# Kernel optimization log

Measured on AMD Instinct MI355X. Metric: run time of the kernel, lower is better.

The kernel has to match this reference:

```python
import jax, jax.numpy as jnp
import numpy as np

DIM = 1024
H_HEADS = 16


def setup_inputs() -> dict:
    key = jax.random.key(0)
    ks = jax.random.split(key, 12)
    h, w = 48, 80
    hw = h * w
    n_frames, n_sel = 11, 384
    wscale = 1.0 / np.sqrt(DIM).astype(np.float32)
    return {
        "feats_cur": jax.random.normal(ks[0], (1, DIM, h, w), jnp.float32),
        "ps": jax.random.normal(ks[1], (1, DIM, h, w), jnp.float32),
        "feats_ref": jax.random.normal(ks[2], (n_frames, DIM, h, w), jnp.float32),
        "ext_mem": jax.random.normal(ks[3], (24000, DIM), jnp.float32),
        "glob_cache": jax.random.normal(ks[4], (4000, DIM), jnp.float32),
        "Wq": jax.random.normal(ks[5], (DIM, DIM), jnp.float32) * wscale,
        "Wk": jax.random.normal(ks[6], (DIM, DIM), jnp.float32) * wscale,
        "Wv": jax.random.normal(ks[7], (DIM, DIM), jnp.float32) * wscale,
        "Wo": jax.random.normal(ks[8], (DIM, DIM), jnp.float32) * wscale,
        "ref_sel_idx": jax.random.randint(ks[9], (n_frames, n_sel), 0, hw, jnp.int32),
        "mem_idx": jax.random.randint(ks[10], (2000,), 0, 24000, jnp.int32),
        "glob_idx": jax.random.randint(ks[11], (2000,), 0, 4000, jnp.int32),
    }


def reference(feats_cur, ps, feats_ref, ext_mem, glob_cache, Wq, Wk, Wv, Wo,
              ref_sel_idx, mem_idx, glob_idx):
    b, dim, h, w = feats_cur.shape
    hw = h * w
    # current-frame pixels with positional encoding -> queries [hw, dim]
    q_in = (feats_cur + ps)[0].reshape(dim, hw).T
    # reference frames + ps -> [F, hw, dim], sparse randperm-style subsample via precomputed indices
    ref = (feats_ref + ps).reshape(-1, dim, hw).transpose(0, 2, 1)
    sel = jnp.take_along_axis(ref, ref_sel_idx[:, :, None], axis=1).reshape(-1, dim)
    # concat with subsampled external memory and global cache pixels
    k_in = jnp.concatenate([sel, ext_mem[mem_idx], glob_cache[glob_idx]], axis=0)  # [Nk, dim]
    dh = dim // H_HEADS
    scale = 1.0 / np.sqrt(dh).astype(np.float32)
    q = (q_in @ Wq).reshape(hw, H_HEADS, dh)
    k = (k_in @ Wk).reshape(-1, H_HEADS, dh)
    v = (k_in @ Wv).reshape(-1, H_HEADS, dh)
    logits = jnp.einsum('qhd,khd->hqk', q, k) * scale  # [H, hw, Nk]
    attn = jax.nn.softmax(logits, axis=-1)
    ctx = jnp.einsum('hqk,khd->qhd', attn, v).reshape(hw, dim)
    out = q_in + ctx @ Wo  # residual, like MEGA relation module
    # back to [1, dim, h, w] as in update_lm_pixel_with_transpose
    return out.T.reshape(1, dim, h, w)
```

## Files before the change

### kernel.cpp

```cpp
#include <hip/hip_runtime.h>

using u16 = unsigned short;
using bf16x8 = __attribute__((ext_vector_type(8))) short;
using f32x4  = __attribute__((ext_vector_type(4))) float;

#define DIM   1024
#define HW    3840
#define NSEL  4224
#define NK    8224
#define NKPAD 8320
#define NH    16
#define THR   50.0f

typedef __attribute__((address_space(1))) const unsigned GU;
typedef __attribute__((address_space(3))) unsigned LU;

__device__ __forceinline__ u16 f2bf(float x) {
    unsigned u = __float_as_uint(x);
    return (u16)((u + 0x7FFFu + ((u >> 16) & 1u)) >> 16);
}

__device__ __forceinline__ float exp2fast(float x) {
    return __builtin_amdgcn_exp2f(x);
}

__global__ void prep_kernel(const float* __restrict__ Wq, const float* __restrict__ Wk,
                            const float* __restrict__ Wv, const float* __restrict__ Wo,
                            const float* __restrict__ fc, const float* __restrict__ ps,
                            const float* __restrict__ fr, const float* __restrict__ em,
                            const float* __restrict__ gc, const int* __restrict__ sel,
                            const int* __restrict__ midx, const int* __restrict__ gidx,
                            u16* __restrict__ WT, u16* __restrict__ qin, u16* __restrict__ kin) {
    const int b = blockIdx.x;
    const int tid = threadIdx.x;
    if (b < 4096) {
        const int zz = b >> 10, yy = (b >> 5) & 31, xx = b & 31;
        const float* src = zz == 0 ? Wq : zz == 1 ? Wk : zz == 2 ? Wv : Wo;
        u16* dst = WT + (size_t)zz * DIM * DIM;
        __shared__ float t[32][33];
        const int n0 = xx * 32, k0 = yy * 32;
        const int tx = tid & 31, ty = tid >> 5;
#pragma unroll
        for (int j = 0; j < 4; ++j)
            t[ty + 8 * j][tx] = src[(size_t)(k0 + ty + 8 * j) * DIM + n0 + tx];
        __syncthreads();
#pragma unroll
        for (int j = 0; j < 4; ++j)
            dst[(size_t)(n0 + ty + 8 * j) * DIM + k0 + tx] = f2bf(t[tx][ty + 8 * j]);
    } else if (b < 7936) {
        const int bb = b - 4096;
        const int xx = bb % 120, yy = bb / 120;
        __shared__ float t[32][33];
        const int p0 = xx * 32, d0 = yy * 32;
        const int tx = tid & 31, ty = tid >> 5;
#pragma unroll
        for (int j = 0; j < 4; ++j) {
            int d = d0 + ty + 8 * j;
            t[ty + 8 * j][tx] = fc[(size_t)d * HW + p0 + tx] + ps[(size_t)d * HW + p0 + tx];
        }
        __syncthreads();
#pragma unroll
        for (int j = 0; j < 4; ++j)
            qin[(size_t)(p0 + ty + 8 * j) * DIM + d0 + tx] = f2bf(t[tx][ty + 8 * j]);
    } else {
        const int row = b - 7936;
        u16* dst = kin + (size_t)row * DIM;
        const int t = tid;
        if (row < NSEL) {
            const int f = row / 384;
            const int idx = sel[row];
            const float* base = fr + (size_t)f * DIM * HW + idx;
#pragma unroll
            for (int j = 0; j < 4; ++j) {
                int d = t + 256 * j;
                dst[d] = f2bf(base[(size_t)d * HW] + ps[(size_t)d * HW + idx]);
            }
        } else if (row < NSEL + 2000) {
            const float* src = em + (size_t)midx[row - NSEL] * DIM;
#pragma unroll
            for (int j = 0; j < 4; ++j) { int d = t + 256 * j; dst[d] = f2bf(src[d]); }
        } else if (row < NK) {
            const float* src = gc + (size_t)gidx[row - (NSEL + 2000)] * DIM;
#pragma unroll
            for (int j = 0; j < 4; ++j) { int d = t + 256 * j; dst[d] = f2bf(src[d]); }
        } else {
#pragma unroll
            for (int j = 0; j < 4; ++j) dst[t + 256 * j] = 0;
        }
    }
}

__device__ __forceinline__ void gemm_bt_body(const u16* __restrict__ A,
                                             const u16* __restrict__ B,
                                             void* __restrict__ Cout,
                                             const float* __restrict__ r1,
                                             const float* __restrict__ r2,
                                             int ldc, int mode, float scale,
                                             int bx, int by) {
    __shared__ __align__(16) u16 As[2][128 * 64];
    __shared__ __align__(16) u16 Bs[2][128 * 64];
    const int tid = threadIdx.x;
    const int l = tid & 63;
    const int wv = tid >> 6;
    const int wr = (wv >> 1) * 64, wc = (wv & 1) * 64;
    const int g = l >> 4, lo = l & 15;
    const size_t bm = (size_t)by * 128, bn = (size_t)bx * 128;
    const f32x4 fzero = {0.f, 0.f, 0.f, 0.f};

    f32x4 acc[4][4];
#pragma unroll
    for (int i = 0; i < 4; ++i)
#pragma unroll
        for (int j = 0; j < 4; ++j) acc[i][j] = fzero;

#define GSTAGE(BUF, KT)                                                                         \
    {                                                                                           \
        const int k0_ = (KT) * 64;                                                              \
        _Pragma("unroll") for (int q = 0; q < 4; ++q) {                                         \
            const int idx = q * 256 + tid;                                                      \
            const int row = idx >> 3, c8 = idx & 7;                                             \
            const int scol = (c8 ^ (row & 7)) * 8;                                              \
            const int dbase = q * 2048 + wv * 512;                                              \
            __builtin_amdgcn_global_load_lds((GU*)(A + (bm + row) * DIM + k0_ + scol),          \
                                             (LU*)&As[BUF][dbase], 16, 0, 0);                   \
            __builtin_amdgcn_global_load_lds((GU*)(B + (bn + row) * DIM + k0_ + scol),          \
                                             (LU*)&Bs[BUF][dbase], 16, 0, 0);                   \
        }                                                                                       \
    }

#define GCOMPUTE(BUF)                                                                           \
    {                                                                                           \
        _Pragma("unroll") for (int ks = 0; ks < 2; ++ks) {                                      \
            bf16x8 af[4], bfv[4];                                                               \
            _Pragma("unroll") for (int mi = 0; mi < 4; ++mi) {                                  \
                const int row = wr + mi * 16 + lo;                                              \
                const int sw = (ks * 4 + g) ^ (row & 7);                                        \
                af[mi] = *(const bf16x8*)(&As[BUF][row * 64 + sw * 8]);                         \
            }                                                                                   \
            _Pragma("unroll") for (int ni = 0; ni < 4; ++ni) {                                  \
                const int row = wc + ni * 16 + lo;                                              \
                const int sw = (ks * 4 + g) ^ (row & 7);                                        \
                bfv[ni] = *(const bf16x8*)(&Bs[BUF][row * 64 + sw * 8]);                        \
            }                                                                                   \
            _Pragma("unroll") for (int mi = 0; mi < 4; ++mi)                                    \
                _Pragma("unroll") for (int ni = 0; ni < 4; ++ni)                                \
                    acc[mi][ni] = __builtin_amdgcn_mfma_f32_16x16x32_bf16(af[mi], bfv[ni], acc[mi][ni], 0, 0, 0); \
        }                                                                                       \
    }

    GSTAGE(0, 0)
    asm volatile("s_waitcnt vmcnt(0)" ::: "memory");
    __syncthreads();

#pragma unroll 1
    for (int kt = 0; kt < 16; kt += 2) {
        GSTAGE(1, kt + 1)
        GCOMPUTE(0)
        asm volatile("s_waitcnt vmcnt(0)" ::: "memory");
        __syncthreads();
        if (kt + 2 < 16) GSTAGE(0, kt + 2)
        GCOMPUTE(1)
        asm volatile("s_waitcnt vmcnt(0)" ::: "memory");
        __syncthreads();
    }
#undef GCOMPUTE
#undef GSTAGE

    if (mode == 0) {
        u16* C = (u16*)Cout;
#pragma unroll
        for (int mi = 0; mi < 4; ++mi)
#pragma unroll
            for (int ni = 0; ni < 4; ++ni)
#pragma unroll
                for (int r = 0; r < 4; ++r) {
                    size_t m = bm + wr + mi * 16 + g * 4 + r;
                    size_t n = bn + wc + ni * 16 + lo;
                    C[m * (size_t)ldc + n] = f2bf(acc[mi][ni][r] * scale);
                }
    } else if (mode == 2) {
        u16* C = (u16*)Cout;
#pragma unroll
        for (int mi = 0; mi < 4; ++mi)
#pragma unroll
            for (int ni = 0; ni < 4; ++ni)
#pragma unroll
                for (int r = 0; r < 4; ++r) {
                    size_t m = bm + wr + mi * 16 + g * 4 + r;
                    size_t n = bn + wc + ni * 16 + lo;
                    size_t o = (n >> 6) * ((size_t)NKPAD * 64) + m * 64 + (n & 63);
                    C[o] = f2bf(acc[mi][ni][r] * scale);
                }
    } else {
        float* C = (float*)Cout;
#pragma unroll
        for (int mi = 0; mi < 4; ++mi)
#pragma unroll
            for (int ni = 0; ni < 4; ++ni)
#pragma unroll
                for (int r = 0; r < 4; ++r) {
                    size_t m = bm + wr + mi * 16 + g * 4 + r;
                    size_t n = bn + wc + ni * 16 + lo;
                    size_t o = m * (size_t)ldc + n;
                    C[o] = acc[mi][ni][r] + r1[o] + r2[o];
                }
    }
}

__global__ __launch_bounds__(256, 2) void proj_kernel(const u16* __restrict__ qin,
                                                      const u16* __restrict__ kin,
                                                      const u16* __restrict__ WT,
                                                      u16* __restrict__ Qp,
                                                      u16* __restrict__ Kp,
                                                      u16* __restrict__ Vt) {
    const int b = blockIdx.x;
    if (b < 240) {
        gemm_bt_body(qin, WT, Qp, nullptr, nullptr, 1024, 0, 0.18033688f, b % 8, b / 8);
    } else if (b < 760) {
        const int bb = b - 240;
        gemm_bt_body(kin, WT + 1048576, Kp, nullptr, nullptr, 1024, 2, 1.0f, bb % 8, bb / 8);
    } else {
        const int bb = b - 760;
        gemm_bt_body(WT + 2097152, kin, Vt, nullptr, nullptr, NKPAD, 0, 1.0f, bb % 65, bb / 65);
    }
}

__global__ __launch_bounds__(256, 2) void outproj_kernel(const u16* __restrict__ WTo,
                                                         const u16* __restrict__ ctx,
                                                         float* __restrict__ out,
                                                         const float* __restrict__ fc,
                                                         const float* __restrict__ ps) {
    gemm_bt_body(WTo, ctx, out, fc, ps, HW, 1, 1.0f, blockIdx.x, blockIdx.y);
}

__global__ __launch_bounds__(256, 4) void attn_kernel(const u16* __restrict__ Q,
                                                      const u16* __restrict__ Kh,
                                                      const u16* __restrict__ Vt,
                                                      u16* __restrict__ ctx) {
    __shared__ __align__(16) u16 Kst[2][2][2048];
    __shared__ __align__(16) u16 Vst[2][2][2048];
    __shared__ float mlb[2][2][32][2];
    __shared__ float mbuf2[2][32][20];
    const int h = blockIdx.x;
    const int tid = threadIdx.x;
    const int l = tid & 63, wv = tid >> 6;
    const int qh = wv & 1, kh = wv >> 1;
    const int g = l >> 4, lo = l & 15;
    const int hoff = h * 64;
    const int qw = blockIdx.y * 64 + qh * 32;
    const f32x4 fzero = {0.f, 0.f, 0.f, 0.f};
    const int sig = (lo >> 2) * 8 + (lo & 3);
    const int W0 = kh * 128;
    const int nw = 128 + kh;

    const u16* Ksrc = Kh + (size_t)h * NKPAD * 64;
    const u16* Vsrc = Vt + (size_t)hoff * NKPAD;

    bf16x8 qa[2][2];
#pragma unroll
    for (int mi = 0; mi < 2; ++mi)
#pragma unroll
        for (int ks = 0; ks < 2; ++ks)
            qa[mi][ks] = *(const bf16x8*)(Q + (size_t)(qw + mi * 16 + lo) * DIM + hoff + ks * 32 + g * 8);

    f32x4 acc[2][4];
#pragma unroll
    for (int mi = 0; mi < 2; ++mi)
#pragma unroll
        for (int ni = 0; ni < 4; ++ni) acc[mi][ni] = fzero;
    float mrow[2] = {-1e30f, -1e30f};
    float lsum[2] = {0.f, 0.f};
    float pmax[2] = {-1e30f, -1e30f};

#define STAGE32(BUF, IT)                                                                        \
    {                                                                                           \
        const int kk_ = (W0 + (IT)) * 32;                                                       \
        _Pragma("unroll") for (int jj = 0; jj < 2; ++jj) {                                      \
            const int j = qh * 2 + jj;                                                          \
            const int rk = j * 8 + (l >> 3);                                                    \
            const int hkk = (rk & 3) | (((rk >> 3) & 1) << 2);                                  \
            const u16* gK = Ksrc + (size_t)(kk_ + rk) * 64 + (((l & 7) ^ hkk) * 8);             \
            __builtin_amdgcn_global_load_lds((GU*)gK, (LU*)&Kst[kh][BUF][j * 512], 16, 0, 0);   \
            const int xu = (l & 7) ^ (l >> 3);                                                  \
            const int dv = 2 * rk + (xu >> 2);                                                  \
            const u16* gV = Vsrc + (size_t)dv * NKPAD + kk_ + ((xu & 3) * 8);                   \
            __builtin_amdgcn_global_load_lds((GU*)gV, (LU*)&Vst[kh][BUF][j * 512], 16, 0, 0);   \
        }                                                                                       \
    }

#define COMPUTE32(BUF)                                                                          \
    {                                                                                           \
        bf16x8 kf0, kf1, kf2, kf3;                                                              \
        {                                                                                       \
            const int r0_ = sig, r1_ = sig + 4;                                                 \
            const int h0_ = (r0_ & 3) | (((r0_ >> 3) & 1) << 2);                                \
            const int h1_ = (r1_ & 3) | (((r1_ >> 3) & 1) << 2);                                \
            kf0 = *(const bf16x8*)(&Kst[kh][BUF][r0_ * 64 + ((0 + g) ^ h0_) * 8]);              \
            kf1 = *(const bf16x8*)(&Kst[kh][BUF][r0_ * 64 + ((4 + g) ^ h0_) * 8]);              \
            kf2 = *(const bf16x8*)(&Kst[kh][BUF][r1_ * 64 + ((0 + g) ^ h1_) * 8]);              \
            kf3 = *(const bf16x8*)(&Kst[kh][BUF][r1_ * 64 + ((4 + g) ^ h1_) * 8]);              \
        }                                                                                       \
        f32x4 S0[2], S1[2];                                                                     \
        _Pragma("unroll") for (int mi = 0; mi < 2; ++mi) {                                      \
            f32x4 s_ = __builtin_amdgcn_mfma_f32_16x16x32_bf16(kf0, qa[mi][0], fzero, 0, 0, 0); \
            S0[mi] = __builtin_amdgcn_mfma_f32_16x16x32_bf16(kf1, qa[mi][1], s_, 0, 0, 0);      \
            f32x4 t_ = __builtin_amdgcn_mfma_f32_16x16x32_bf16(kf2, qa[mi][0], fzero, 0, 0, 0); \
            S1[mi] = __builtin_amdgcn_mfma_f32_16x16x32_bf16(kf3, qa[mi][1], t_, 0, 0, 0);      \
        }                                                                                       \
        _Pragma("unroll") for (int mi = 0; mi < 2; ++mi) {                                      \
            float a_ = fmaxf(fmaxf(S0[mi][0], S0[mi][1]), fmaxf(S0[mi][2], S0[mi][3]));         \
            float b_ = fmaxf(fmaxf(S1[mi][0], S1[mi][1]), fmaxf(S1[mi][2], S1[mi][3]));         \
            pmax[mi] = fmaxf(pmax[mi], fmaxf(a_, b_));                                          \
        }                                                                                       \
        if (__any(fmaxf(pmax[0] - mrow[0], pmax[1] - mrow[1]) > THR)) {                         \
            _Pragma("unroll") for (int mi = 0; mi < 2; ++mi) {                                  \
                float v = pmax[mi];                                                             \
                v = fmaxf(v, __shfl_xor(v, 16));                                                \
                v = fmaxf(v, __shfl_xor(v, 32));                                                \
                float mn = fmaxf(mrow[mi], v);                                                  \
                float fct = exp2fast(mrow[mi] - mn);                                            \
                mrow[mi] = mn;                                                                  \
                lsum[mi] *= fct;                                                                \
                _Pragma("unroll") for (int r = 0; r < 4; ++r) {                                 \
                    float fr_ = __shfl(fct, g * 4 + r);                                         \
                    _Pragma("unroll") for (int ni = 0; ni < 4; ++ni) acc[mi][ni][r] *= fr_;     \
                }                                                                               \
            }                                                                                   \
        }                                                                                       \
        bf16x8 vb[4];                                                                           \
        _Pragma("unroll") for (int ni = 0; ni < 4; ++ni) {                                      \
            const int R_ = ni * 8 + (lo >> 1);                                                  \
            const int ck_ = (((lo & 1) * 4 + g) ^ (lo >> 1)) * 8;                               \
            vb[ni] = *(const bf16x8*)(&Vst[kh][BUF][R_ * 64 + ck_]);                            \
        }                                                                                       \
        _Pragma("unroll") for (int mi = 0; mi < 2; ++mi) {                                      \
            float p0 = exp2fast(S0[mi][0] - mrow[mi]);                                          \
            float p1 = exp2fast(S0[mi][1] - mrow[mi]);                                          \
            float p2 = exp2fast(S0[mi][2] - mrow[mi]);                                          \
            float p3 = exp2fast(S0[mi][3] - mrow[mi]);                                          \
            float p4 = exp2fast(S1[mi][0] - mrow[mi]);                                          \
            float p5 = exp2fast(S1[mi][1] - mrow[mi]);                                          \
            float p6 = exp2fast(S1[mi][2] - mrow[mi]);                                          \
            float p7 = exp2fast(S1[mi][3] - mrow[mi]);                                          \
            lsum[mi] += ((p0 + p1) + (p2 + p3)) + ((p4 + p5) + (p6 + p7));                      \
            union { unsigned u[4]; bf16x8 v; } pu;                                              \
            asm("v_cvt_pk_bf16_f32 %0, %1, %2" : "=v"(pu.u[0]) : "v"(p0), "v"(p1));             \
            asm("v_cvt_pk_bf16_f32 %0, %1, %2" : "=v"(pu.u[1]) : "v"(p2), "v"(p3));             \
            asm("v_cvt_pk_bf16_f32 %0, %1, %2" : "=v"(pu.u[2]) : "v"(p4), "v"(p5));             \
            asm("v_cvt_pk_bf16_f32 %0, %1, %2" : "=v"(pu.u[3]) : "v"(p6), "v"(p7));             \
            _Pragma("unroll") for (int ni = 0; ni < 4; ++ni)                                    \
                acc[mi][ni] = __builtin_amdgcn_mfma_f32_16x16x32_bf16(pu.v, vb[ni], acc[mi][ni], 0, 0, 0); \
        }                                                                                       \
    }

    STAGE32(0, 0)
    asm volatile("s_waitcnt vmcnt(0)" ::: "memory");
    __syncthreads();

#pragma unroll 1
    for (int it = 0; it + 1 < nw; it += 2) {
        STAGE32(1, it + 1)
        COMPUTE32(0)
        asm volatile("s_waitcnt vmcnt(0)" ::: "memory");
        __syncthreads();
        STAGE32(0, it + 2)
        COMPUTE32(1)
        asm volatile("s_waitcnt vmcnt(0)" ::: "memory");
        __syncthreads();
    }
    if (kh == 1) {
        COMPUTE32(0)
    }
#undef COMPUTE32
#undef STAGE32

#pragma unroll
    for (int mi = 0; mi < 2; ++mi) {
        float t = lsum[mi];
        t += __shfl_xor(t, 16);
        t += __shfl_xor(t, 32);
        lsum[mi] = t;
    }
    if (l < 16) {
        mlb[kh][qh][lo][0] = mrow[0];
        mlb[kh][qh][lo][1] = lsum[0];
        mlb[kh][qh][16 + lo][0] = mrow[1];
        mlb[kh][qh][16 + lo][1] = lsum[1];
    }
    __syncthreads();

    float esf[2][4], inl[2][4];
#pragma unroll
    for (int mi = 0; mi < 2; ++mi)
#pragma unroll
        for (int r = 0; r < 4; ++r) {
            const int row = mi * 16 + g * 4 + r;
            float m0 = mlb[0][qh][row][0], l0 = mlb[0][qh][row][1];
            float m1 = mlb[1][qh][row][0], l1 = mlb[1][qh][row][1];
            float M = fmaxf(m0, m1);
            float e0 = exp2fast(m0 - M), e1 = exp2fast(m1 - M);
            esf[mi][r] = kh ? e1 : e0;
            inl[mi][r] = 1.0f / (l0 * e0 + l1 * e1);
        }

#pragma unroll
    for (int ni = 0; ni < 4; ++ni) {
        __syncthreads();
        if (kh == 1) {
#pragma unroll
            for (int mi = 0; mi < 2; ++mi)
#pragma unroll
                for (int r = 0; r < 4; ++r)
                    mbuf2[qh][mi * 16 + g * 4 + r][lo] = acc[mi][ni][r] * esf[mi][r];
        }
        __syncthreads();
        if (kh == 0) {
#pragma unroll
            for (int mi = 0; mi < 2; ++mi)
#pragma unroll
                for (int r = 0; r < 4; ++r) {
                    float val = (acc[mi][ni][r] * esf[mi][r] + mbuf2[qh][mi * 16 + g * 4 + r][lo]) * inl[mi][r];
                    ctx[(size_t)(qw + mi * 16 + g * 4 + r) * DIM + hoff + ni * 16 + lo] = f2bf(val);
                }
        }
    }
}

extern "C" void kernel_launch(void* const* d_in, const int* in_sizes, int n_in,
                              void* d_out, int out_size, void* d_ws, size_t ws_size,
                              hipStream_t stream) {
    const float* fc  = (const float*)d_in[0];
    const float* ps  = (const float*)d_in[1];
    const float* fr  = (const float*)d_in[2];
    const float* em  = (const float*)d_in[3];
    const float* gc  = (const float*)d_in[4];
    const float* Wq  = (const float*)d_in[5];
    const float* Wk  = (const float*)d_in[6];
    const float* Wv  = (const float*)d_in[7];
    const float* Wo  = (const float*)d_in[8];
    const int* sel   = (const int*)d_in[9];
    const int* midx  = (const int*)d_in[10];
    const int* gidx  = (const int*)d_in[11];

    char* w = (char*)d_ws;
    u16* WT  = (u16*)(w);
    u16* qin = (u16*)(w + 8388608ull);
    u16* kin = (u16*)(w + 16252928ull);
    u16* Qp  = (u16*)(w + 33292288ull);
    u16* Kp  = (u16*)(w + 41156608ull);
    u16* Vt  = (u16*)(w + 58195968ull);
    u16* ctx = (u16*)(w + 75235328ull);
    float* out = (float*)d_out;

    prep_kernel<<<dim3(16256), dim3(256), 0, stream>>>(Wq, Wk, Wv, Wo, fc, ps, fr, em, gc,
                                                       sel, midx, gidx, WT, qin, kin);
    proj_kernel<<<dim3(1280), dim3(256), 0, stream>>>(qin, kin, WT, Qp, Kp, Vt);

    attn_kernel<<<dim3(NH, 60), dim3(256), 0, stream>>>(Qp, Kp, Vt, ctx);

    outproj_kernel<<<dim3(30, 8), dim3(256), 0, stream>>>(WT + 3145728, ctx, out, fc, ps);
}
```

Measured before the change: 421.3 us.

## Load V fragments directly from global into registers and widen K stages

New measurement: 733.9 us. 1.74x slower.

```diff
diff --git a/kernel.cpp b/kernel.cpp
--- a/kernel.cpp
+++ b/kernel.cpp
@@ -237,8 +237,7 @@
                                                       const u16* __restrict__ Kh,
                                                       const u16* __restrict__ Vt,
                                                       u16* __restrict__ ctx) {
-    __shared__ __align__(16) u16 Kst[2][2][2048];
-    __shared__ __align__(16) u16 Vst[2][2][2048];
+    __shared__ __align__(16) u16 Kst[2][2][4096];
     __shared__ float mlb[2][2][32][2];
     __shared__ float mbuf2[2][32][20];
     const int h = blockIdx.x;
@@ -250,8 +249,6 @@
     const int qw = blockIdx.y * 64 + qh * 32;
     const f32x4 fzero = {0.f, 0.f, 0.f, 0.f};
     const int sig = (lo >> 2) * 8 + (lo & 3);
-    const int W0 = kh * 128;
-    const int nw = 128 + kh;
 
     const u16* Ksrc = Kh + (size_t)h * NKPAD * 64;
     const u16* Vsrc = Vt + (size_t)hoff * NKPAD;
@@ -272,27 +269,30 @@
     float lsum[2] = {0.f, 0.f};
     float pmax[2] = {-1e30f, -1e30f};
 
-#define STAGE32(BUF, IT)                                                                        \
+#define KSTAGE(BUF, IT)                                                                         \
     {                                                                                           \
-        const int kk_ = (W0 + (IT)) * 32;                                                       \
-        _Pragma("unroll") for (int jj = 0; jj < 2; ++jj) {                                      \
-            const int j = qh * 2 + jj;                                                          \
-            const int rk = j * 8 + (l >> 3);                                                    \
-            const int hkk = (rk & 3) | (((rk >> 3) & 1) << 2);                                  \
-            const u16* gK = Ksrc + (size_t)(kk_ + rk) * 64 + (((l & 7) ^ hkk) * 8);             \
-            __builtin_amdgcn_global_load_lds((GU*)gK, (LU*)&Kst[kh][BUF][j * 512], 16, 0, 0);   \
-            const int xu = (l & 7) ^ (l >> 3);                                                  \
-            const int dv = 2 * rk + (xu >> 2);                                                  \
-            const u16* gV = Vsrc + (size_t)dv * NKPAD + kk_ + ((xu & 3) * 8);                   \
-            __builtin_amdgcn_global_load_lds((GU*)gV, (LU*)&Vst[kh][BUF][j * 512], 16, 0, 0);   \
-        }                                                                                       \
-    }
-
-#define COMPUTE32(BUF)                                                                          \
+        const size_t kk_ = (size_t)(kh * 64 + (IT)) * 64;                                       \
+        _Pragma("unroll") for (int j = 0; j < 4; ++j) {                                         \
+            const int inst = qh * 4 + j;                                                        \
+            const int rk = inst * 8 + (l >> 3);                                                 \
+            const int hkk = ((l >> 3) & 3) | ((inst & 1) << 2);                                 \
+            const u16* gK = Ksrc + (kk_ + rk) * 64 + (((l & 7) ^ hkk) * 8);                     \
+            __builtin_amdgcn_global_load_lds((GU*)gK, (LU*)&Kst[kh][BUF][inst * 512], 16, 0, 0);\
+        }                                                                                       \
+    }
+
+#define VHALF(VR, IT, S)                                                                        \
+    {                                                                                           \
+        const size_t kb_ = (size_t)(kh * 64 + (IT)) * 64 + (S) * 32 + g * 8;                    \
+        _Pragma("unroll") for (int ni = 0; ni < 4; ++ni)                                        \
+            VR[ni] = *(const bf16x8*)(Vsrc + (size_t)(ni * 16 + lo) * NKPAD + kb_);             \
+    }
+
+#define CHALF(BUF, S, VR)                                                                       \
     {                                                                                           \
         bf16x8 kf0, kf1, kf2, kf3;                                                              \
         {                                                                                       \
-            const int r0_ = sig, r1_ = sig + 4;                                                 \
+            const int r0_ = (S) * 32 + sig, r1_ = (S) * 32 + 4 + sig;                           \
             const int h0_ = (r0_ & 3) | (((r0_ >> 3) & 1) << 2);                                \
             const int h1_ = (r1_ & 3) | (((r1_ >> 3) & 1) << 2);                                \
             kf0 = *(const bf16x8*)(&Kst[kh][BUF][r0_ * 64 + ((0 + g) ^ h0_) * 8]);              \
@@ -326,12 +326,6 @@
                     _Pragma("unroll") for (int ni = 0; ni < 4; ++ni) acc[mi][ni][r] *= fr_;     \
                 }                                                                               \
             }                                                                                   \
-        }                                                                                       \
-        bf16x8 vb[4];                                                                           \
-        _Pragma("unroll") for (int ni = 0; ni < 4; ++ni) {                                      \
-            const int R_ = ni * 8 + (lo >> 1);                                                  \
-            const int ck_ = (((lo & 1) * 4 + g) ^ (lo >> 1)) * 8;                               \
-            vb[ni] = *(const bf16x8*)(&Vst[kh][BUF][R_ * 64 + ck_]);                            \
         }                                                                                       \
         _Pragma("unroll") for (int mi = 0; mi < 2; ++mi) {                                      \
             float p0 = exp2fast(S0[mi][0] - mrow[mi]);                                          \
@@ -349,30 +343,39 @@
             asm("v_cvt_pk_bf16_f32 %0, %1, %2" : "=v"(pu.u[2]) : "v"(p4), "v"(p5));             \
             asm("v_cvt_pk_bf16_f32 %0, %1, %2" : "=v"(pu.u[3]) : "v"(p6), "v"(p7));             \
             _Pragma("unroll") for (int ni = 0; ni < 4; ++ni)                                    \
-                acc[mi][ni] = __builtin_amdgcn_mfma_f32_16x16x32_bf16(pu.v, vb[ni], acc[mi][ni], 0, 0, 0); \
-        }                                                                                       \
-    }
-
-    STAGE32(0, 0)
+                acc[mi][ni] = __builtin_amdgcn_mfma_f32_16x16x32_bf16(pu.v, VR[ni], acc[mi][ni], 0, 0, 0); \
+        }                                                                                       \
+    }
+
+    bf16x8 vA[4], vB[4];
+    KSTAGE(0, 0)
+    VHALF(vA, 0, 0)
     asm volatile("s_waitcnt vmcnt(0)" ::: "memory");
     __syncthreads();
 
 #pragma unroll 1
-    for (int it = 0; it + 1 < nw; it += 2) {
-        STAGE32(1, it + 1)
-        COMPUTE32(0)
+    for (int it = 0; it < 64; it += 2) {
+        KSTAGE(1, it + 1)
+        VHALF(vB, it, 1)
+        CHALF(0, 0, vA)
+        VHALF(vA, it + 1, 0)
+        CHALF(0, 1, vB)
         asm volatile("s_waitcnt vmcnt(0)" ::: "memory");
         __syncthreads();
-        STAGE32(0, it + 2)
-        COMPUTE32(1)
+        KSTAGE(0, it + 2)
+        VHALF(vB, it + 1, 1)
+        CHALF(1, 0, vA)
+        VHALF(vA, it + 2, 0)
+        CHALF(1, 1, vB)
         asm volatile("s_waitcnt vmcnt(0)" ::: "memory");
         __syncthreads();
     }
     if (kh == 1) {
-        COMPUTE32(0)
-    }
-#undef COMPUTE32
-#undef STAGE32
+        CHALF(0, 0, vA)
+    }
+#undef CHALF
+#undef VHALF
+#undef KSTAGE
 
 #pragma unroll
     for (int mi = 0; mi < 2; ++mi) {
```
